# Kernel tuning notes

Hardware: AMD Instinct MI355X
Metric: run time of the kernel (lower is better)

Reference implementation:

```python
import jax, jax.numpy as jnp
import numpy as np

N_HEADS = 8
OUT_DIM = 64
LEAKY_SLOPE = 0.2


def setup_inputs() -> dict:
    key = jax.random.key(0)
    k1, k2, k3 = jax.random.split(key, 3)
    N, IN_DIM = 4096, 256
    x = jax.random.normal(k1, (N, IN_DIM), dtype=jnp.float32)
    # nn.Linear(in_dim, out_dim*n_heads, bias=False): weight shape (out*heads, in)
    W = jax.random.normal(k2, (OUT_DIM * N_HEADS, IN_DIM), dtype=jnp.float32) * (1.0 / np.sqrt(IN_DIM))
    # attention vector, xavier-ish scale
    attn = jax.random.normal(k3, (1, N_HEADS, 2 * OUT_DIM), dtype=jnp.float32) * 0.1
    return {"x": x, "W": W, "attn": attn}


def reference(x, W, attn):
    N = x.shape[0]
    # Wx: (N, H, D)
    Wx = (x @ W.T).reshape(N, N_HEADS, OUT_DIM)
    # The torch code concats src/tgt then dots with attn; this decomposes exactly:
    # e[i,j,h] = leaky_relu( Wx[i,h]·a_src[h] + Wx[j,h]·a_tgt[h] )
    a_src = attn[0, :, :OUT_DIM]   # (H, D)
    a_tgt = attn[0, :, OUT_DIM:]   # (H, D)
    s = jnp.einsum('nhd,hd->nh', Wx, a_src)  # (N, H) score of row index (src)
    t = jnp.einsum('nhd,hd->nh', Wx, a_tgt)  # (N, H) score of col index (tgt)
    e = jax.nn.leaky_relu(s[:, None, :] + t[None, :, :], LEAKY_SLOPE)  # (N, N, H)
    a = jax.nn.softmax(e, axis=1)  # softmax over dim=1 (neighbors j)
    # out[i,h,d] = sum_j a[i,j,h] * Wx[j,h,d]
    out = jnp.einsum('ijh,jhd->ihd', a, Wx)
    return out.reshape(N, N_HEADS * OUT_DIM)  # concat=True
```

## Files before the change

kernel.cpp:

```cpp
#include <hip/hip_runtime.h>
#include <hip/hip_bf16.h>

#define NN 4096
#define KD 256
#define NH 8
#define DD 64
#define HD 512
#define SLOPE 0.2f
#define NSLICE 16
#define SLEN 256

__global__ __launch_bounds__(256) void gemm_st(const float* __restrict__ x,
                                               const float* __restrict__ W,
                                               const float* __restrict__ attn,
                                               float* __restrict__ Wx,
                                               float* __restrict__ sH,
                                               float* __restrict__ tH) {
    const int h  = blockIdx.x;
    const int bn = h * 64;
    const int bm = blockIdx.y * 64;
    __shared__ float As[16][68];
    __shared__ float Bs[16][68];
    const int tid = threadIdx.x;
    const int tx = tid & 15, ty = tid >> 4;
    const int lr = tid >> 2;
    const int lk = (tid & 3) * 4;
    float acc[4][4] = {};
    for (int k0 = 0; k0 < KD; k0 += 16) {
        float4 av = *(const float4*)&x[(bm + lr) * KD + k0 + lk];
        float4 bv = *(const float4*)&W[(bn + lr) * KD + k0 + lk];
        __syncthreads();
        As[lk + 0][lr] = av.x; As[lk + 1][lr] = av.y;
        As[lk + 2][lr] = av.z; As[lk + 3][lr] = av.w;
        Bs[lk + 0][lr] = bv.x; Bs[lk + 1][lr] = bv.y;
        Bs[lk + 2][lr] = bv.z; Bs[lk + 3][lr] = bv.w;
        __syncthreads();
#pragma unroll
        for (int kk = 0; kk < 16; ++kk) {
            float4 a = *(const float4*)&As[kk][ty * 4];
            float4 b = *(const float4*)&Bs[kk][tx * 4];
            acc[0][0] += a.x * b.x; acc[0][1] += a.x * b.y; acc[0][2] += a.x * b.z; acc[0][3] += a.x * b.w;
            acc[1][0] += a.y * b.x; acc[1][1] += a.y * b.y; acc[1][2] += a.y * b.z; acc[1][3] += a.y * b.w;
            acc[2][0] += a.z * b.x; acc[2][1] += a.z * b.y; acc[2][2] += a.z * b.z; acc[2][3] += a.z * b.w;
            acc[3][0] += a.w * b.x; acc[3][1] += a.w * b.y; acc[3][2] += a.w * b.z; acc[3][3] += a.w * b.w;
        }
    }
#pragma unroll
    for (int m = 0; m < 4; ++m)
#pragma unroll
        for (int n = 0; n < 4; ++n)
            Wx[(bm + ty * 4 + m) * HD + bn + tx * 4 + n] = acc[m][n];
    float4 as4 = *(const float4*)&attn[h * 128 + tx * 4];
    float4 at4 = *(const float4*)&attn[h * 128 + 64 + tx * 4];
#pragma unroll
    for (int m = 0; m < 4; ++m) {
        float s = acc[m][0] * as4.x + acc[m][1] * as4.y + acc[m][2] * as4.z + acc[m][3] * as4.w;
        float t = acc[m][0] * at4.x + acc[m][1] * at4.y + acc[m][2] * at4.z + acc[m][3] * at4.w;
#pragma unroll
        for (int off = 1; off < 16; off <<= 1) {
            s += __shfl_xor(s, off, 16);
            t += __shfl_xor(t, off, 16);
        }
        if (tx == 0) {
            sH[h * NN + bm + ty * 4 + m] = s;
            tH[h * NN + bm + ty * 4 + m] = t;
        }
    }
}

__global__ __launch_bounds__(256) void count_partial(const float* __restrict__ tH,
                                                     const float* __restrict__ sH,
                                                     int* __restrict__ partialR,
                                                     int* __restrict__ partialC) {
    const int h = blockIdx.y;
    const int slice = blockIdx.z;
    const int j = blockIdx.x * 256 + threadIdx.x;
    __shared__ float tl[SLEN];
    tl[threadIdx.x] = tH[h * NN + slice * SLEN + threadIdx.x];
    __syncthreads();
    const float myT  = tH[h * NN + j];
    const float negS = -sH[h * NN + j];
    const int pbase = slice * SLEN;
    int r = 0, cs = 0;
#pragma unroll 8
    for (int p = 0; p < SLEN; ++p) {
        float v = tl[p];
        r  += (v < myT) | ((v == myT) & ((pbase + p) < j));
        cs += (v <= negS);
    }
    partialR[(h * NSLICE + slice) * NN + j] = r;
    partialC[(h * NSLICE + slice) * NN + j] = cs;
}

__global__ __launch_bounds__(256) void scatter_kernel(const float* __restrict__ tH,
                                                      const int* __restrict__ partialR,
                                                      const int* __restrict__ partialC,
                                                      int* __restrict__ sortedIdx,
                                                      float* __restrict__ expT,
                                                      float* __restrict__ expT2,
                                                      int* __restrict__ cIdx) {
    const int h = blockIdx.y;
    const int j = blockIdx.x * 256 + threadIdx.x;
    int r = 0, cs = 0;
#pragma unroll
    for (int s = 0; s < NSLICE; ++s) {
        r  += partialR[(h * NSLICE + s) * NN + j];
        cs += partialC[(h * NSLICE + s) * NN + j];
    }
    const float myT = tH[h * NN + j];
    sortedIdx[h * NN + r] = j;
    expT[h * NN + r]      = expf(myT);
    expT2[h * NN + r]     = expf(SLOPE * myT);
    cIdx[h * NN + j]      = cs;
}

__global__ __launch_bounds__(256) void local_prefix(const float* __restrict__ Wx,
                                                    const int* __restrict__ sortedIdx,
                                                    const float* __restrict__ expT,
                                                    const float* __restrict__ expT2,
                                                    float* __restrict__ localW,
                                                    float* __restrict__ localW2,
                                                    float* __restrict__ chunkTotW,
                                                    float* __restrict__ chunkTotW2,
                                                    float* __restrict__ localZ,
                                                    float* __restrict__ localZ2,
                                                    float* __restrict__ chunkZtot,
                                                    float* __restrict__ chunkZtot2) {
    const int c = blockIdx.x, h = blockIdx.y;
    const int tid = threadIdx.x;
    const int wid = tid >> 6, d = tid & 63;
    const int base = h * NN + c * 64;
    __shared__ float sums[4][64], sums2[4][64];
    float run = 0.f, run2 = 0.f;
    float ex[16], ex2[16];
#pragma unroll
    for (int kk = 0; kk < 16; ++kk) {
        int k = wid * 16 + kk;
        int j = sortedIdx[base + k];
        float w  = expT[base + k];
        float w2 = expT2[base + k];
        float v = Wx[j * HD + h * DD + d];
        ex[kk]  = run;  run  += w  * v;
        ex2[kk] = run2; run2 += w2 * v;
    }
    sums[wid][d] = run; sums2[wid][d] = run2;
    __syncthreads();
    float off = 0.f, off2 = 0.f;
    for (int w = 0; w < 4; ++w) {
        if (w < wid) { off += sums[w][d]; off2 += sums2[w][d]; }
    }
#pragma unroll
    for (int kk = 0; kk < 16; ++kk) {
        int k = wid * 16 + kk;
        localW [(h * NN + c * 64 + k) * 64 + d] = ex[kk]  + off;
        localW2[(h * NN + c * 64 + k) * 64 + d] = ex2[kk] + off2;
    }
    if (wid == 3) {
        chunkTotW [(h * 64 + c) * 64 + d] = off  + run;
        chunkTotW2[(h * 64 + c) * 64 + d] = off2 + run2;
    }
    if (wid == 0) {
        float z0 = expT[base + d];
        float z = z0;
#pragma unroll
        for (int o = 1; o < 64; o <<= 1) { float n = __shfl_up(z, o, 64); if (d >= o) z += n; }
        localZ[h * NN + c * 64 + d] = z - z0;
        if (d == 63) chunkZtot[h * 64 + c] = z;
    } else if (wid == 1) {
        float z0 = expT2[base + d];
        float z = z0;
#pragma unroll
        for (int o = 1; o < 64; o <<= 1) { float n = __shfl_up(z, o, 64); if (d >= o) z += n; }
        localZ2[h * NN + c * 64 + d] = z - z0;
        if (d == 63) chunkZtot2[h * 64 + c] = z;
    }
}

__global__ __launch_bounds__(256) void chunk_scan(float* __restrict__ chunkTotW,
                                                  float* __restrict__ chunkTotW2,
                                                  float* __restrict__ chunkZtot,
                                                  float* __restrict__ chunkZtot2,
                                                  float* __restrict__ totW,
                                                  float* __restrict__ totW2,
                                                  float* __restrict__ Ztot,
                                                  float* __restrict__ Ztot2) {
    const int h = blockIdx.x;
    const int tid = threadIdx.x;
    const int lane = tid & 63;
    __shared__ float cw[64 * 64];
    __shared__ float cw2[64 * 64];
    __shared__ float zb[64], zb2[64];
#pragma unroll
    for (int it = 0; it < 16; ++it) {
        int lin = it * 256 + tid;
        cw[lin]  = chunkTotW [h * 4096 + lin];
        cw2[lin] = chunkTotW2[h * 4096 + lin];
    }
    if (tid >= 128 && tid < 192) zb[lane]  = chunkZtot [h * 64 + lane];
    if (tid >= 192)              zb2[lane] = chunkZtot2[h * 64 + lane];
    __syncthreads();
    if (tid < 64) {
        float acc = 0.f;
        for (int c = 0; c < 64; ++c) { int idx = c * 64 + tid; float t = cw[idx]; cw[idx] = acc; acc += t; }
        totW[h * 64 + tid] = acc;
    } else if (tid < 128) {
        int d = tid - 64;
        float acc = 0.f;
        for (int c = 0; c < 64; ++c) { int idx = c * 64 + d; float t = cw2[idx]; cw2[idx] = acc; acc += t; }
        totW2[h * 64 + d] = acc;
    } else if (tid < 192) {
        float z0 = zb[lane];
        float z = z0;
#pragma unroll
        for (int o = 1; o < 64; o <<= 1) { float n = __shfl_up(z, o, 64); if (lane >= o) z += n; }
        chunkZtot[h * 64 + lane] = z - z0;
        if (lane == 63) Ztot[h] = z;
    } else {
        float z0 = zb2[lane];
        float z = z0;
#pragma unroll
        for (int o = 1; o < 64; o <<= 1) { float n = __shfl_up(z, o, 64); if (lane >= o) z += n; }
        chunkZtot2[h * 64 + lane] = z - z0;
        if (lane == 63) Ztot2[h] = z;
    }
    __syncthreads();
#pragma unroll
    for (int it = 0; it < 16; ++it) {
        int lin = it * 256 + tid;
        chunkTotW [h * 4096 + lin] = cw[lin];
        chunkTotW2[h * 4096 + lin] = cw2[lin];
    }
}

__global__ __launch_bounds__(256) void out_kernel(const float* __restrict__ sH,
                                                  const int* __restrict__ cIdx,
                                                  const float* __restrict__ localW,
                                                  const float* __restrict__ localW2,
                                                  const float* __restrict__ chunkTotW,
                                                  const float* __restrict__ chunkTotW2,
                                                  const float* __restrict__ localZ,
                                                  const float* __restrict__ localZ2,
                                                  const float* __restrict__ chunkZtot,
                                                  const float* __restrict__ chunkZtot2,
                                                  const float* __restrict__ totW,
                                                  const float* __restrict__ totW2,
                                                  const float* __restrict__ Ztot,
                                                  const float* __restrict__ Ztot2,
                                                  float* __restrict__ out) {
    const int h = blockIdx.y;
    const int i = blockIdx.x * 4 + (threadIdx.x >> 6);
    const int d = threadIdx.x & 63;
    const float sv = sH[h * NN + i];
    const int c = cIdx[h * NN + i];
    const float es  = expf(sv);
    const float es2 = expf(SLOPE * sv);
    float wpos, wneg, zp, zn;
    if (c == NN) {
        wpos = 0.f; zp = 0.f;
        wneg = totW2[h * 64 + d];
        zn   = Ztot2[h];
    } else {
        float pw  = localW [(h * NN + c) * 64 + d] + chunkTotW [(h * 64 + (c >> 6)) * 64 + d];
        float pw2 = localW2[(h * NN + c) * 64 + d] + chunkTotW2[(h * 64 + (c >> 6)) * 64 + d];
        wpos = totW[h * 64 + d] - pw;
        wneg = pw2;
        float pz  = localZ [h * NN + c] + chunkZtot [h * 64 + (c >> 6)];
        float pz2 = localZ2[h * NN + c] + chunkZtot2[h * 64 + (c >> 6)];
        zp = Ztot[h] - pz;
        zn = pz2;
    }
    out[i * HD + h * DD + d] = (es * wpos + es2 * wneg) / (es * zp + es2 * zn);
}

extern "C" void kernel_launch(void* const* d_in, const int* in_sizes, int n_in,
                              void* d_out, int out_size, void* d_ws, size_t ws_size,
                              hipStream_t stream) {
    const float* x    = (const float*)d_in[0];
    const float* W    = (const float*)d_in[1];
    const float* attn = (const float*)d_in[2];
    float* out = (float*)d_out;

    float* ws = (float*)d_ws;
    size_t o = 0;
    float* Wx        = ws + o; o += (size_t)NN * HD;
    float* sH        = ws + o; o += (size_t)NH * NN;
    float* tH        = ws + o; o += (size_t)NH * NN;
    float* expT      = ws + o; o += (size_t)NH * NN;
    float* expT2     = ws + o; o += (size_t)NH * NN;
    int*   sortedIdx = (int*)(ws + o); o += (size_t)NH * NN;
    int*   cIdx      = (int*)(ws + o); o += (size_t)NH * NN;
    float* localZ    = ws + o; o += (size_t)NH * NN;
    float* localZ2   = ws + o; o += (size_t)NH * NN;
    float* chunkTotW  = ws + o; o += (size_t)NH * 64 * 64;
    float* chunkTotW2 = ws + o; o += (size_t)NH * 64 * 64;
    float* chunkZtot  = ws + o; o += (size_t)NH * 64;
    float* chunkZtot2 = ws + o; o += (size_t)NH * 64;
    float* totW   = ws + o; o += (size_t)NH * 64;
    float* totW2  = ws + o; o += (size_t)NH * 64;
    float* Ztot   = ws + o; o += 64;
    float* Ztot2  = ws + o; o += 64;
    float* localW  = ws + o; o += (size_t)NH * NN * 64;
    float* localW2 = ws + o; o += (size_t)NH * NN * 64;
    int* partialR = (int*)localW;
    int* partialC = (int*)localW2;

    gemm_st<<<dim3(NH, NN / 64), dim3(256), 0, stream>>>(x, W, attn, Wx, sH, tH);
    count_partial<<<dim3(NN / 256, NH, NSLICE), dim3(256), 0, stream>>>(tH, sH, partialR, partialC);
    scatter_kernel<<<dim3(NN / 256, NH), dim3(256), 0, stream>>>(tH, partialR, partialC, sortedIdx, expT, expT2, cIdx);
    local_prefix<<<dim3(64, NH), dim3(256), 0, stream>>>(Wx, sortedIdx, expT, expT2, localW, localW2,
                                                         chunkTotW, chunkTotW2, localZ, localZ2, chunkZtot, chunkZtot2);
    chunk_scan<<<dim3(NH), dim3(256), 0, stream>>>(chunkTotW, chunkTotW2, chunkZtot, chunkZtot2,
                                                   totW, totW2, Ztot, Ztot2);
    out_kernel<<<dim3(NN / 4, NH), dim3(256), 0, stream>>>(sH, cIdx, localW, localW2, chunkTotW, chunkTotW2,
                                                           localZ, localZ2, chunkZtot, chunkZtot2,
                                                           totW, totW2, Ztot, Ztot2, out);
}
```

Before: 74.17 us.

## Widen GEMM k-tile, vectorize stores, and specialize rank counting by slice position

The GEMM now stages 32-wide k-tiles with two float4 loads per operand and writes Wx with float4 stores, which halves the number of sync points. The rank-counting kernel uses 8 slices of 512 elements instead of 16 of 256. It reads shared memory as float4 and splits into three branches, so the index tie-break comparison runs only on the diagonal slice. Partial counts are stored as unsigned short, which halves the traffic to scatter_kernel, and they still fit because each slice is at most 512. These are several independent micro-optimizations across two kernels; the larger shared tiles may reduce occupancy.

```diff
diff --git a/kernel.cpp b/kernel.cpp
--- a/kernel.cpp
+++ b/kernel.cpp
@@ -7,8 +7,8 @@
 #define DD 64
 #define HD 512
 #define SLOPE 0.2f
-#define NSLICE 16
-#define SLEN 256
+#define NSLICE 8
+#define SLEN 512
 
 __global__ __launch_bounds__(256) void gemm_st(const float* __restrict__ x,
                                                const float* __restrict__ W,
@@ -19,24 +19,30 @@
     const int h  = blockIdx.x;
     const int bn = h * 64;
     const int bm = blockIdx.y * 64;
-    __shared__ float As[16][68];
-    __shared__ float Bs[16][68];
+    __shared__ float As[32][68];
+    __shared__ float Bs[32][68];
     const int tid = threadIdx.x;
     const int tx = tid & 15, ty = tid >> 4;
-    const int lr = tid >> 2;
-    const int lk = (tid & 3) * 4;
+    const int srow = tid >> 2;
+    const int skq  = (tid & 3) * 8;
     float acc[4][4] = {};
-    for (int k0 = 0; k0 < KD; k0 += 16) {
-        float4 av = *(const float4*)&x[(bm + lr) * KD + k0 + lk];
-        float4 bv = *(const float4*)&W[(bn + lr) * KD + k0 + lk];
+    for (int k0 = 0; k0 < KD; k0 += 32) {
+        float4 a0 = *(const float4*)&x[(bm + srow) * KD + k0 + skq];
+        float4 a1 = *(const float4*)&x[(bm + srow) * KD + k0 + skq + 4];
+        float4 b0 = *(const float4*)&W[(bn + srow) * KD + k0 + skq];
+        float4 b1 = *(const float4*)&W[(bn + srow) * KD + k0 + skq + 4];
         __syncthreads();
-        As[lk + 0][lr] = av.x; As[lk + 1][lr] = av.y;
-        As[lk + 2][lr] = av.z; As[lk + 3][lr] = av.w;
-        Bs[lk + 0][lr] = bv.x; Bs[lk + 1][lr] = bv.y;
-        Bs[lk + 2][lr] = bv.z; Bs[lk + 3][lr] = bv.w;
+        As[skq + 0][srow] = a0.x; As[skq + 1][srow] = a0.y;
+        As[skq + 2][srow] = a0.z; As[skq + 3][srow] = a0.w;
+        As[skq + 4][srow] = a1.x; As[skq + 5][srow] = a1.y;
+        As[skq + 6][srow] = a1.z; As[skq + 7][srow] = a1.w;
+        Bs[skq + 0][srow] = b0.x; Bs[skq + 1][srow] = b0.y;
+        Bs[skq + 2][srow] = b0.z; Bs[skq + 3][srow] = b0.w;
+        Bs[skq + 4][srow] = b1.x; Bs[skq + 5][srow] = b1.y;
+        Bs[skq + 6][srow] = b1.z; Bs[skq + 7][srow] = b1.w;
         __syncthreads();
 #pragma unroll
-        for (int kk = 0; kk < 16; ++kk) {
+        for (int kk = 0; kk < 32; ++kk) {
             float4 a = *(const float4*)&As[kk][ty * 4];
             float4 b = *(const float4*)&Bs[kk][tx * 4];
             acc[0][0] += a.x * b.x; acc[0][1] += a.x * b.y; acc[0][2] += a.x * b.z; acc[0][3] += a.x * b.w;
@@ -47,9 +53,7 @@
     }
 #pragma unroll
     for (int m = 0; m < 4; ++m)
-#pragma unroll
-        for (int n = 0; n < 4; ++n)
-            Wx[(bm + ty * 4 + m) * HD + bn + tx * 4 + n] = acc[m][n];
+        *(float4*)&Wx[(bm + ty * 4 + m) * HD + bn + tx * 4] = *(const float4*)&acc[m][0];
     float4 as4 = *(const float4*)&attn[h * 128 + tx * 4];
     float4 at4 = *(const float4*)&attn[h * 128 + 64 + tx * 4];
 #pragma unroll
@@ -70,31 +74,53 @@
 
 __global__ __launch_bounds__(256) void count_partial(const float* __restrict__ tH,
                                                      const float* __restrict__ sH,
-                                                     int* __restrict__ partialR,
-                                                     int* __restrict__ partialC) {
+                                                     unsigned short* __restrict__ partialR,
+                                                     unsigned short* __restrict__ partialC) {
     const int h = blockIdx.y;
     const int slice = blockIdx.z;
-    const int j = blockIdx.x * 256 + threadIdx.x;
+    const int jb = blockIdx.x;
+    const int j = jb * 256 + threadIdx.x;
     __shared__ float tl[SLEN];
-    tl[threadIdx.x] = tH[h * NN + slice * SLEN + threadIdx.x];
+    for (int p = threadIdx.x; p < SLEN; p += 256) tl[p] = tH[h * NN + slice * SLEN + p];
     __syncthreads();
     const float myT  = tH[h * NN + j];
     const float negS = -sH[h * NN + j];
-    const int pbase = slice * SLEN;
+    const float4* tl4 = (const float4*)tl;
     int r = 0, cs = 0;
-#pragma unroll 8
-    for (int p = 0; p < SLEN; ++p) {
-        float v = tl[p];
-        r  += (v < myT) | ((v == myT) & ((pbase + p) < j));
-        cs += (v <= negS);
-    }
-    partialR[(h * NSLICE + slice) * NN + j] = r;
-    partialC[(h * NSLICE + slice) * NN + j] = cs;
+    if (slice == (jb >> 1)) {
+        const int pbase = slice * SLEN;
+#pragma unroll 4
+        for (int p4 = 0; p4 < SLEN / 4; ++p4) {
+            float4 v = tl4[p4];
+            int p = pbase + p4 * 4;
+            r += (v.x < myT) | ((v.x == myT) & ((p + 0) < j));
+            r += (v.y < myT) | ((v.y == myT) & ((p + 1) < j));
+            r += (v.z < myT) | ((v.z == myT) & ((p + 2) < j));
+            r += (v.w < myT) | ((v.w == myT) & ((p + 3) < j));
+            cs += (v.x <= negS) + (v.y <= negS) + (v.z <= negS) + (v.w <= negS);
+        }
+    } else if (slice < (jb >> 1)) {
+#pragma unroll 4
+        for (int p4 = 0; p4 < SLEN / 4; ++p4) {
+            float4 v = tl4[p4];
+            r  += (v.x <= myT) + (v.y <= myT) + (v.z <= myT) + (v.w <= myT);
+            cs += (v.x <= negS) + (v.y <= negS) + (v.z <= negS) + (v.w <= negS);
+        }
+    } else {
+#pragma unroll 4
+        for (int p4 = 0; p4 < SLEN / 4; ++p4) {
+            float4 v = tl4[p4];
+            r  += (v.x < myT) + (v.y < myT) + (v.z < myT) + (v.w < myT);
+            cs += (v.x <= negS) + (v.y <= negS) + (v.z <= negS) + (v.w <= negS);
+        }
+    }
+    partialR[(h * NSLICE + slice) * NN + j] = (unsigned short)r;
+    partialC[(h * NSLICE + slice) * NN + j] = (unsigned short)cs;
 }
 
 __global__ __launch_bounds__(256) void scatter_kernel(const float* __restrict__ tH,
-                                                      const int* __restrict__ partialR,
-                                                      const int* __restrict__ partialC,
+                                                      const unsigned short* __restrict__ partialR,
+                                                      const unsigned short* __restrict__ partialC,
                                                       int* __restrict__ sortedIdx,
                                                       float* __restrict__ expT,
                                                       float* __restrict__ expT2,
@@ -301,8 +327,8 @@
     float* Ztot2  = ws + o; o += 64;
     float* localW  = ws + o; o += (size_t)NH * NN * 64;
     float* localW2 = ws + o; o += (size_t)NH * NN * 64;
-    int* partialR = (int*)localW;
-    int* partialC = (int*)localW2;
+    unsigned short* partialR = (unsigned short*)localW;
+    unsigned short* partialC = (unsigned short*)localW2;
 
     gemm_st<<<dim3(NH, NN / 64), dim3(256), 0, stream>>>(x, W, attn, Wx, sH, tH);
     count_partial<<<dim3(NN / 256, NH, NSLICE), dim3(256), 0, stream>>>(tH, sH, partialR, partialC);
```

Result: no change. 72.97 us (-1.6%).
